# Kernel tuning notes

Measured on AMD Instinct MI355X. Metric: run time of the kernel, lower is better.

The kernel has to match this reference:

```python
import jax, jax.numpy as jnp
import numpy as np

HILBERT_BITS = 8
NDIM = 3


def hilbert_distance(grid, bits=HILBERT_BITS):
    """Vectorized Skilling transform: grid [..., 3] int32 in [0, 2**bits-1] -> Hilbert index [...] int32.
    Exact port of hilbertcurve.HilbertCurve.distance_from_point (n=3, p=bits)."""
    x = [grid[..., i] for i in range(NDIM)]
    m = 1 << (bits - 1)
    # Inverse undo excess work
    q = m
    while q > 1:
        pm = q - 1
        for i in range(NDIM):
            cond = (x[i] & q) != 0
            if i == 0:
                x[0] = jnp.where(cond, x[0] ^ pm, x[0])
            else:
                t = (x[0] ^ x[i]) & pm
                x0n = jnp.where(cond, x[0] ^ pm, x[0] ^ t)
                xin = jnp.where(cond, x[i], x[i] ^ t)
                x[0], x[i] = x0n, xin
        q >>= 1
    # Gray encode
    x[1] = x[1] ^ x[0]
    x[2] = x[2] ^ x[1]
    t = jnp.zeros_like(x[2])
    q = m
    while q > 1:
        t = jnp.where((x[2] & q) != 0, t ^ (q - 1), t)
        q >>= 1
    x = [xi ^ t for xi in x]
    # Interleave bits, MSB first, dim order 0,1,2 -> h has bits*3 bits (24 fits int32)
    h = jnp.zeros_like(x[0])
    for bpos in range(bits - 1, -1, -1):
        for i in range(NDIM):
            h = (h << 1) | ((x[i] >> bpos) & 1)
    return h


def hilbert_orders(x, bits=HILBERT_BITS):
    # x: [B, N, 3] float. Per-batch min/max normalization, then quantize to grid.
    mins = x.min(axis=1, keepdims=True)
    maxs = x.max(axis=1, keepdims=True)
    span = jnp.maximum(maxs - mins, 1e-6)
    norm = (x - mins) / span
    mx = (1 << bits) - 1
    grid_h = jnp.clip(norm * mx, 0, mx).astype(jnp.int32)
    grid_t = jnp.clip(norm[..., ::-1] * mx, 0, mx).astype(jnp.int32)  # [z,y,x] variant
    order_h = jnp.argsort(hilbert_distance(grid_h, bits), axis=-1)
    order_t = jnp.argsort(hilbert_distance(grid_t, bits), axis=-1)
    return order_h, order_t


def setup_inputs() -> dict:
    key = jax.random.key(0)
    k1, k2, k3 = jax.random.split(key, 3)
    B, N, D = 16, 4096, 384
    x = jax.random.normal(k1, (B, N, 3), dtype=jnp.float32)
    W = jax.random.normal(k2, (D, 3), dtype=jnp.float32) * 0.5
    b = jax.random.normal(k3, (D,), dtype=jnp.float32) * 0.1
    gamma = jnp.ones((2, D), dtype=jnp.float32)
    beta = jnp.zeros((2, D), dtype=jnp.float32)
    return {"x": x, "W": W, "b": b, "gamma": gamma, "beta": beta}


def reference(x, W, b, gamma, beta):
    order_h, order_t = hilbert_orders(x)                     # [B, N] each
    pts_h = jnp.take_along_axis(x, order_h[..., None], axis=1)  # [B, N, 3]
    pts_t = jnp.take_along_axis(x, order_t[..., None], axis=1)
    base_h = jnp.einsum('bnc,dc->bnd', pts_h, W) + b         # Linear(3, D)
    base_t = jnp.einsum('bnc,dc->bnd', pts_t, W) + b
    tokens_h = base_h * gamma[0] + beta[0]
    tokens_t = base_t * gamma[1] + beta[1]
    return jnp.concatenate([tokens_h, tokens_t], axis=1)     # [B, 2N, D]
```

## Files before the change

### kernel.cpp

```cpp
#include <hip/hip_runtime.h>
#include <stdint.h>

#define BATCH 16
#define NPTS 4096
#define DIM 384
#define NTOK (2*NPTS)
#define F4PT (DIM/4)

typedef unsigned long long u64;

__device__ __forceinline__ uint32_t spread3(uint32_t x) {
    x = (x | (x << 8)) & 0x00F00Fu;
    x = (x | (x << 4)) & 0x0C30C3u;
    x = (x | (x << 2)) & 0x249249u;
    return x;
}

__device__ __forceinline__ uint32_t hilbert3(uint32_t x0, uint32_t x1, uint32_t x2) {
    #pragma unroll
    for (uint32_t q = 128; q > 1; q >>= 1) {
        uint32_t pm = q - 1;
        if (x0 & q) x0 ^= pm;
        uint32_t t = (x0 ^ x1) & pm;
        if (x1 & q) { x0 ^= pm; } else { x0 ^= t; x1 ^= t; }
        t = (x0 ^ x2) & pm;
        if (x2 & q) { x0 ^= pm; } else { x0 ^= t; x2 ^= t; }
    }
    x1 ^= x0;
    x2 ^= x1;
    uint32_t t = 0;
    #pragma unroll
    for (uint32_t q = 128; q > 1; q >>= 1) { if (x2 & q) t ^= (q - 1); }
    x0 ^= t; x1 ^= t; x2 ^= t;
    return (spread3(x0) << 2) | (spread3(x1) << 1) | spread3(x2);
}

__global__ __launch_bounds__(512) void order_radix_o(const float* __restrict__ x,
                                                     u64* __restrict__ kws) {
    const int bi = blockIdx.x;
    const int b = bi >> 4;
    const int v = (bi >> 3) & 1;
    const int oct = bi & 7;
    const int t = threadIdx.x;
    const int lane = t & 63;
    const int w = t >> 6;

    __shared__ u64 skey[512];
    __shared__ uint32_t hist[6 * 128];
    __shared__ uint32_t baseArr[16];
    __shared__ float red[8 * 6];

    const float* xb = x + (size_t)b * NPTS * 3;
    const float4* xb4 = (const float4*)xb;

    float mnx = 1e30f, mny = 1e30f, mnz = 1e30f;
    float mxx = -1e30f, mxy = -1e30f, mxz = -1e30f;
    #pragma unroll
    for (int h = 0; h < 2; ++h) {
        float4 q0 = xb4[h * 1536 + 3 * t + 0];
        float4 q1 = xb4[h * 1536 + 3 * t + 1];
        float4 q2 = xb4[h * 1536 + 3 * t + 2];
        float px[4] = {q0.x, q0.w, q1.z, q2.y};
        float py[4] = {q0.y, q1.x, q1.w, q2.z};
        float pz[4] = {q0.z, q1.y, q2.x, q2.w};
        #pragma unroll
        for (int r = 0; r < 4; ++r) {
            mnx = fminf(mnx, px[r]); mxx = fmaxf(mxx, px[r]);
            mny = fminf(mny, py[r]); mxy = fmaxf(mxy, py[r]);
            mnz = fminf(mnz, pz[r]); mxz = fmaxf(mxz, pz[r]);
        }
    }
    #pragma unroll
    for (int off = 32; off > 0; off >>= 1) {
        mnx = fminf(mnx, __shfl_xor(mnx, off));
        mny = fminf(mny, __shfl_xor(mny, off));
        mnz = fminf(mnz, __shfl_xor(mnz, off));
        mxx = fmaxf(mxx, __shfl_xor(mxx, off));
        mxy = fmaxf(mxy, __shfl_xor(mxy, off));
        mxz = fmaxf(mxz, __shfl_xor(mxz, off));
    }
    if (lane == 0) {
        red[w*6+0] = mnx; red[w*6+1] = mny; red[w*6+2] = mnz;
        red[w*6+3] = mxx; red[w*6+4] = mxy; red[w*6+5] = mxz;
    }
    hist[t] = 0u;
    if (t < 256) hist[512 + t] = 0u;
    __syncthreads();
    if (t == 0) {
        for (int ww = 1; ww < 8; ++ww) {
            mnx = fminf(mnx, red[ww*6+0]); mny = fminf(mny, red[ww*6+1]);
            mnz = fminf(mnz, red[ww*6+2]); mxx = fmaxf(mxx, red[ww*6+3]);
            mxy = fmaxf(mxy, red[ww*6+4]); mxz = fmaxf(mxz, red[ww*6+5]);
        }
        red[0] = mnx; red[1] = mny; red[2] = mnz;
        red[3] = fmaxf(mxx - mnx, 1e-6f);
        red[4] = fmaxf(mxy - mny, 1e-6f);
        red[5] = fmaxf(mxz - mnz, 1e-6f);
    }
    __syncthreads();
    mnx = red[0]; mny = red[1]; mnz = red[2];
    const float spx = red[3], spy = red[4], spz = red[5];

    u64 key;
    {
        const int n0 = (oct << 9) + t;
        float cx = xb[3*n0+0], cy = xb[3*n0+1], cz = xb[3*n0+2];
        float gx = fminf(fmaxf(((cx - mnx) / spx) * 255.0f, 0.0f), 255.0f);
        float gy = fminf(fmaxf(((cy - mny) / spy) * 255.0f, 0.0f), 255.0f);
        float gz = fminf(fmaxf(((cz - mnz) / spz) * 255.0f, 0.0f), 255.0f);
        uint32_t ix = (uint32_t)(int)gx;
        uint32_t iy = (uint32_t)(int)gy;
        uint32_t iz = (uint32_t)(int)gz;
        uint32_t a0 = v ? iz : ix;
        uint32_t a2 = v ? ix : iz;
        uint32_t code = hilbert3(a0, iy, a2);
        key = ((u64)code << 12) | (u64)n0;
    }

    const u64 below_mask = (1ull << lane) - 1ull;
    u64* segk = kws + (((b << 1) | v) << 12);

    #pragma unroll
    for (int p = 0; p < 6; ++p) {
        const int sh = 12 + 4 * p;
        uint32_t* histp = hist + p * 128;

        unsigned d = (unsigned)(key >> sh) & 15u;
        u64 m = ~0ull;
        #pragma unroll
        for (int bit = 0; bit < 4; ++bit) {
            u64 bal = __ballot((int)((d >> bit) & 1u));
            m &= ((d >> bit) & 1u) ? bal : ~bal;
        }
        unsigned rk = (unsigned)__popcll(m & below_mask);
        if (rk == 0u)
            histp[d * 8 + w] = (unsigned)__popcll(m);
        __syncthreads();

        if (t < 16) {
            unsigned running = 0;
            #pragma unroll
            for (int s = 0; s < 8; ++s) {
                unsigned hv = histp[t * 8 + s];
                histp[t * 8 + s] = running;
                running += hv;
            }
            unsigned tv = running;
            #pragma unroll
            for (int off = 1; off < 16; off <<= 1) {
                unsigned nv = __shfl_up(tv, off);
                if (lane >= off) tv += nv;
            }
            baseArr[t] = tv - running;
        }
        __syncthreads();

        unsigned pos = baseArr[d] + histp[d * 8 + w] + rk;

        if (p < 5) {
            skey[pos] = key;
            __syncthreads();
            key = skey[t];
        } else {
            segk[(oct << 9) + pos] = key;
        }
    }
}

__global__ __launch_bounds__(512) void merge_emit_kernel(const float* __restrict__ x,
                                                         const float* __restrict__ W,
                                                         const float* __restrict__ bias,
                                                         const float* __restrict__ gamma,
                                                         const float* __restrict__ beta,
                                                         const u64* __restrict__ kws,
                                                         float4* __restrict__ out4) {
    const int bi = blockIdx.x;
    const int b = bi >> 4;
    const int v = (bi >> 3) & 1;
    const int oct = bi & 7;
    const int t = threadIdx.x;

    __shared__ u64 runs[8 * 512];
    __shared__ __align__(16) float sw0[DIM], sw1[DIM], sw2[DIM], sc[DIM];
    __shared__ float cxs[512], cys[512], czs[512];
    __shared__ int rnk[512];

    if (t < DIM) {
        float g = gamma[v * DIM + t];
        sw0[t] = g * W[t*3+0];
        sw1[t] = g * W[t*3+1];
        sw2[t] = g * W[t*3+2];
        sc[t]  = g * bias[t] + beta[v * DIM + t];
    }

    const u64* segk = kws + (((b << 1) | v) << 12);
    #pragma unroll
    for (int j = 0; j < 8; ++j)
        runs[(j << 9) + t] = segk[(j << 9) + t];
    __syncthreads();

    u64 k = runs[(oct << 9) + t];
    int base7[7], c[7];
    #pragma unroll
    for (int j = 0; j < 7; ++j) {
        base7[j] = (j + (j >= oct ? 1 : 0)) << 9;
        c[j] = 0;
    }
    #pragma unroll
    for (int step = 512; step >= 1; step >>= 1) {
        #pragma unroll
        for (int j = 0; j < 7; ++j) {
            if (c[j] + step <= 512 && runs[base7[j] + c[j] + step - 1] < k)
                c[j] += step;
        }
    }
    int rank = t;
    #pragma unroll
    for (int j = 0; j < 7; ++j) rank += c[j];

    {
        int idx = (int)(k & 0xFFFull);
        const float* p = x + (size_t)b * NPTS * 3 + idx * 3;
        cxs[t] = p[0]; cys[t] = p[1]; czs[t] = p[2];
        rnk[t] = rank;
    }
    __syncthreads();

    const int tokbase = (b << 13) + (v << 12);
    for (int i = t; i < 512 * F4PT; i += 512) {
        int r = i / F4PT;
        int g = i - r * F4PT;
        float pxr = cxs[r], pyr = cys[r], pzr = czs[r];
        int d0 = g << 2;
        float4 w0 = *(const float4*)&sw0[d0];
        float4 w1 = *(const float4*)&sw1[d0];
        float4 w2 = *(const float4*)&sw2[d0];
        float4 cc = *(const float4*)&sc[d0];
        float4 o;
        o.x = pxr*w0.x + pyr*w1.x + pzr*w2.x + cc.x;
        o.y = pxr*w0.y + pyr*w1.y + pzr*w2.y + cc.y;
        o.z = pxr*w0.z + pyr*w1.z + pzr*w2.z + cc.z;
        o.w = pxr*w0.w + pyr*w1.w + pzr*w2.w + cc.w;
        out4[(size_t)(tokbase + rnk[r]) * F4PT + g] = o;
    }
}

extern "C" void kernel_launch(void* const* d_in, const int* in_sizes, int n_in,
                              void* d_out, int out_size, void* d_ws, size_t ws_size,
                              hipStream_t stream) {
    const float* x     = (const float*)d_in[0];
    const float* W     = (const float*)d_in[1];
    const float* bias  = (const float*)d_in[2];
    const float* gamma = (const float*)d_in[3];
    const float* beta  = (const float*)d_in[4];

    u64* kws = (u64*)d_ws;

    hipLaunchKernelGGL(order_radix_o,     dim3(BATCH * 16), dim3(512), 0, stream, x, kws);
    hipLaunchKernelGGL(merge_emit_kernel, dim3(BATCH * 16), dim3(512), 0, stream,
                       x, W, bias, gamma, beta, kws, (float4*)d_out);
}
```

Baseline: 50.78 us.

## Fuse radix sort and merge-emit into one cooperative kernel with grid syncs

Merges the two kernels into a single cooperative launch. The per-batch min/max reduction is now split across the 16 blocks of each batch, with partial results written to global memory and combined after a grid sync. A second grid sync replaces the kernel boundary before the merge and emit phase. This removes one launch and the redundant full-batch min/max scan in every block, but adds two grid-wide barriers and higher shared-memory use per block, which may cap occupancy.

```diff
diff --git a/kernel.cpp b/kernel.cpp
--- a/kernel.cpp
+++ b/kernel.cpp
@@ -1,5 +1,8 @@
 #include <hip/hip_runtime.h>
+#include <hip/hip_cooperative_groups.h>
 #include <stdint.h>
+
+namespace cg = cooperative_groups;
 
 #define BATCH 16
 #define NPTS 4096
@@ -35,12 +38,21 @@
     return (spread3(x0) << 2) | (spread3(x1) << 1) | spread3(x2);
 }
 
-__global__ __launch_bounds__(512) void order_radix_o(const float* __restrict__ x,
-                                                     u64* __restrict__ kws) {
+__global__ __launch_bounds__(512) void fused_kernel(const float* __restrict__ x,
+                                                    const float* __restrict__ W,
+                                                    const float* __restrict__ bias,
+                                                    const float* __restrict__ gamma,
+                                                    const float* __restrict__ beta,
+                                                    u64* __restrict__ kws,
+                                                    float* __restrict__ partials,
+                                                    float4* __restrict__ out4) {
+    cg::grid_group grid = cg::this_grid();
+
     const int bi = blockIdx.x;
     const int b = bi >> 4;
     const int v = (bi >> 3) & 1;
     const int oct = bi & 7;
+    const int slice = bi & 15;
     const int t = threadIdx.x;
     const int lane = t & 63;
     const int w = t >> 6;
@@ -49,57 +61,70 @@
     __shared__ uint32_t hist[6 * 128];
     __shared__ uint32_t baseArr[16];
     __shared__ float red[8 * 6];
+    __shared__ u64 runs[8 * 512];
+    __shared__ __align__(16) float sw0[DIM], sw1[DIM], sw2[DIM], sc[DIM];
+    __shared__ float cxs[512], cys[512], czs[512];
+    __shared__ int rnk[512];
 
     const float* xb = x + (size_t)b * NPTS * 3;
-    const float4* xb4 = (const float4*)xb;
+
+    {
+        float mnx = 1e30f, mny = 1e30f, mnz = 1e30f;
+        float mxx = -1e30f, mxy = -1e30f, mxz = -1e30f;
+        if (t < 256) {
+            int n = (slice << 8) + t;
+            float cx = xb[3*n+0], cy = xb[3*n+1], cz = xb[3*n+2];
+            mnx = cx; mxx = cx; mny = cy; mxy = cy; mnz = cz; mxz = cz;
+        }
+        #pragma unroll
+        for (int off = 32; off > 0; off >>= 1) {
+            mnx = fminf(mnx, __shfl_xor(mnx, off));
+            mny = fminf(mny, __shfl_xor(mny, off));
+            mnz = fminf(mnz, __shfl_xor(mnz, off));
+            mxx = fmaxf(mxx, __shfl_xor(mxx, off));
+            mxy = fmaxf(mxy, __shfl_xor(mxy, off));
+            mxz = fmaxf(mxz, __shfl_xor(mxz, off));
+        }
+        if (lane == 0) {
+            red[w*6+0] = mnx; red[w*6+1] = mny; red[w*6+2] = mnz;
+            red[w*6+3] = mxx; red[w*6+4] = mxy; red[w*6+5] = mxz;
+        }
+        __syncthreads();
+        if (t == 0) {
+            for (int ww = 1; ww < 8; ++ww) {
+                mnx = fminf(mnx, red[ww*6+0]); mny = fminf(mny, red[ww*6+1]);
+                mnz = fminf(mnz, red[ww*6+2]); mxx = fmaxf(mxx, red[ww*6+3]);
+                mxy = fmaxf(mxy, red[ww*6+4]); mxz = fmaxf(mxz, red[ww*6+5]);
+            }
+            float* pp = partials + bi * 6;
+            pp[0] = mnx; pp[1] = mny; pp[2] = mnz;
+            pp[3] = mxx; pp[4] = mxy; pp[5] = mxz;
+        }
+        __threadfence();
+    }
+    grid.sync();
+
+    if (t < DIM) {
+        float g = gamma[v * DIM + t];
+        sw0[t] = g * W[t*3+0];
+        sw1[t] = g * W[t*3+1];
+        sw2[t] = g * W[t*3+2];
+        sc[t]  = g * bias[t] + beta[v * DIM + t];
+    }
+    hist[t] = 0u;
+    if (t < 256) hist[512 + t] = 0u;
 
     float mnx = 1e30f, mny = 1e30f, mnz = 1e30f;
     float mxx = -1e30f, mxy = -1e30f, mxz = -1e30f;
     #pragma unroll
-    for (int h = 0; h < 2; ++h) {
-        float4 q0 = xb4[h * 1536 + 3 * t + 0];
-        float4 q1 = xb4[h * 1536 + 3 * t + 1];
-        float4 q2 = xb4[h * 1536 + 3 * t + 2];
-        float px[4] = {q0.x, q0.w, q1.z, q2.y};
-        float py[4] = {q0.y, q1.x, q1.w, q2.z};
-        float pz[4] = {q0.z, q1.y, q2.x, q2.w};
-        #pragma unroll
-        for (int r = 0; r < 4; ++r) {
-            mnx = fminf(mnx, px[r]); mxx = fmaxf(mxx, px[r]);
-            mny = fminf(mny, py[r]); mxy = fmaxf(mxy, py[r]);
-            mnz = fminf(mnz, pz[r]); mxz = fmaxf(mxz, pz[r]);
-        }
-    }
-    #pragma unroll
-    for (int off = 32; off > 0; off >>= 1) {
-        mnx = fminf(mnx, __shfl_xor(mnx, off));
-        mny = fminf(mny, __shfl_xor(mny, off));
-        mnz = fminf(mnz, __shfl_xor(mnz, off));
-        mxx = fmaxf(mxx, __shfl_xor(mxx, off));
-        mxy = fmaxf(mxy, __shfl_xor(mxy, off));
-        mxz = fmaxf(mxz, __shfl_xor(mxz, off));
-    }
-    if (lane == 0) {
-        red[w*6+0] = mnx; red[w*6+1] = mny; red[w*6+2] = mnz;
-        red[w*6+3] = mxx; red[w*6+4] = mxy; red[w*6+5] = mxz;
-    }
-    hist[t] = 0u;
-    if (t < 256) hist[512 + t] = 0u;
-    __syncthreads();
-    if (t == 0) {
-        for (int ww = 1; ww < 8; ++ww) {
-            mnx = fminf(mnx, red[ww*6+0]); mny = fminf(mny, red[ww*6+1]);
-            mnz = fminf(mnz, red[ww*6+2]); mxx = fmaxf(mxx, red[ww*6+3]);
-            mxy = fmaxf(mxy, red[ww*6+4]); mxz = fmaxf(mxz, red[ww*6+5]);
-        }
-        red[0] = mnx; red[1] = mny; red[2] = mnz;
-        red[3] = fmaxf(mxx - mnx, 1e-6f);
-        red[4] = fmaxf(mxy - mny, 1e-6f);
-        red[5] = fmaxf(mxz - mnz, 1e-6f);
-    }
-    __syncthreads();
-    mnx = red[0]; mny = red[1]; mnz = red[2];
-    const float spx = red[3], spy = red[4], spz = red[5];
+    for (int s = 0; s < 16; ++s) {
+        const float* pp = partials + ((b << 4) + s) * 6;
+        mnx = fminf(mnx, pp[0]); mny = fminf(mny, pp[1]); mnz = fminf(mnz, pp[2]);
+        mxx = fmaxf(mxx, pp[3]); mxy = fmaxf(mxy, pp[4]); mxz = fmaxf(mxz, pp[5]);
+    }
+    const float spx = fmaxf(mxx - mnx, 1e-6f);
+    const float spy = fmaxf(mxy - mny, 1e-6f);
+    const float spz = fmaxf(mxz - mnz, 1e-6f);
 
     u64 key;
     {
@@ -116,6 +141,7 @@
         uint32_t code = hilbert3(a0, iy, a2);
         key = ((u64)code << 12) | (u64)n0;
     }
+    __syncthreads();
 
     const u64 below_mask = (1ull << lane) - 1ull;
     u64* segk = kws + (((b << 1) | v) << 12);
@@ -165,35 +191,9 @@
             segk[(oct << 9) + pos] = key;
         }
     }
-}
-
-__global__ __launch_bounds__(512) void merge_emit_kernel(const float* __restrict__ x,
-                                                         const float* __restrict__ W,
-                                                         const float* __restrict__ bias,
-                                                         const float* __restrict__ gamma,
-                                                         const float* __restrict__ beta,
-                                                         const u64* __restrict__ kws,
-                                                         float4* __restrict__ out4) {
-    const int bi = blockIdx.x;
-    const int b = bi >> 4;
-    const int v = (bi >> 3) & 1;
-    const int oct = bi & 7;
-    const int t = threadIdx.x;
-
-    __shared__ u64 runs[8 * 512];
-    __shared__ __align__(16) float sw0[DIM], sw1[DIM], sw2[DIM], sc[DIM];
-    __shared__ float cxs[512], cys[512], czs[512];
-    __shared__ int rnk[512];
-
-    if (t < DIM) {
-        float g = gamma[v * DIM + t];
-        sw0[t] = g * W[t*3+0];
-        sw1[t] = g * W[t*3+1];
-        sw2[t] = g * W[t*3+2];
-        sc[t]  = g * bias[t] + beta[v * DIM + t];
-    }
-
-    const u64* segk = kws + (((b << 1) | v) << 12);
+    __threadfence();
+    grid.sync();
+
     #pragma unroll
     for (int j = 0; j < 8; ++j)
         runs[(j << 9) + t] = segk[(j << 9) + t];
@@ -220,7 +220,7 @@
 
     {
         int idx = (int)(k & 0xFFFull);
-        const float* p = x + (size_t)b * NPTS * 3 + idx * 3;
+        const float* p = xb + idx * 3;
         cxs[t] = p[0]; cys[t] = p[1]; czs[t] = p[2];
         rnk[t] = rank;
     }
@@ -254,9 +254,12 @@
     const float* gamma = (const float*)d_in[3];
     const float* beta  = (const float*)d_in[4];
 
-    u64* kws = (u64*)d_ws;
-
-    hipLaunchKernelGGL(order_radix_o,     dim3(BATCH * 16), dim3(512), 0, stream, x, kws);
-    hipLaunchKernelGGL(merge_emit_kernel, dim3(BATCH * 16), dim3(512), 0, stream,
-                       x, W, bias, gamma, beta, kws, (float4*)d_out);
-}
+    u64* kws        = (u64*)d_ws;
+    float* partials = (float*)(kws + 32 * 4096);
+    float4* out4    = (float4*)d_out;
+
+    void* args[] = {(void*)&x, (void*)&W, (void*)&bias, (void*)&gamma,
+                    (void*)&beta, (void*)&kws, (void*)&partials, (void*)&out4};
+    hipLaunchCooperativeKernel((const void*)fused_kernel,
+                               dim3(BATCH * 16), dim3(512), args, 0, stream);
+}
```

Measured after the change: 192.7 us. +279.5%, slower.
